# Kernel optimization log

Measured on AMD Instinct MI355X. Metric: run time of the kernel, lower is better.

Reference implementation:

```python
import jax, jax.numpy as jnp
import numpy as np

B, N, C = 4, 2048, 1024
H = 16
D = C // H  # head_dim = 64
SCALE = D ** -0.5


def setup_inputs() -> dict:
    key = jax.random.key(0)
    ks = jax.random.split(key, 5)
    s = 0.02
    return {
        "x": jax.random.normal(ks[0], (B, N, C), dtype=jnp.float32),
        "wq": jax.random.normal(ks[1], (C, C), dtype=jnp.float32) * s,
        "wk": jax.random.normal(ks[2], (C, C), dtype=jnp.float32) * s,
        "wv": jax.random.normal(ks[3], (C, C), dtype=jnp.float32) * s,
        "wo": jax.random.normal(ks[4], (C, C), dtype=jnp.float32) * s,
        "bo": jnp.zeros((C,), dtype=jnp.float32),
    }


def reference(x, wq, wk, wv, wo, bo):
    # nn.Linear: y = x @ W^T (no bias for q/k/v since qkv_bias=False)
    b, n, c = x.shape
    q = (x @ wq.T).reshape(b, n, H, D).transpose(0, 2, 1, 3)  # [B,H,N,D]
    k = (x @ wk.T).reshape(b, n, H, D).transpose(0, 2, 1, 3)
    v = (x @ wv.T).reshape(b, n, H, D).transpose(0, 2, 1, 3)
    q = q * SCALE
    attn = jax.nn.softmax(jnp.einsum("bhnd,bhmd->bhnm", q, k), axis=-1)
    out = jnp.einsum("bhnm,bhmd->bhnd", attn, v)  # [B,H,N,D]
    out = out.transpose(0, 2, 1, 3).reshape(b, n, c)
    return out @ wo.T + bo
```

## Files before the change

kernel.cpp:

```cpp
#include <hip/hip_runtime.h>
#include <hip/hip_bf16.h>
#include <stdint.h>


#define GAS __attribute__((address_space(1)))
#define LAS __attribute__((address_space(3)))

typedef __attribute__((ext_vector_type(8))) short v8s;
typedef __attribute__((ext_vector_type(4))) float v4f;

__device__ __forceinline__ unsigned short f2bf(float f) {
  __hip_bfloat16 h = __float2bfloat16(f);
  return __builtin_bit_cast(unsigned short, h);
}

__device__ __forceinline__ float fexp2(float x) {
#if __has_builtin(__builtin_amdgcn_exp2f)
  return __builtin_amdgcn_exp2f(x);
#else
  return __expf(x * 0.6931471805599453f);
#endif
}

__device__ __forceinline__ void gld_lds16(const void* g, void* l) {
  __builtin_amdgcn_global_load_lds((GAS void*)(uintptr_t)g,
                                   (LAS void*)(uint32_t)(uintptr_t)l,
                                   16, 0, 0);
}

__global__ void cvt_f32_bf16(const float* __restrict__ src,
                             unsigned short* __restrict__ dst, int n4) {
  int i = blockIdx.x * blockDim.x + threadIdx.x;
  const int stride = gridDim.x * blockDim.x;
  for (; i < n4; i += stride) {
    float4 f = ((const float4*)src)[i];
    ushort4 u;
    u.x = f2bf(f.x); u.y = f2bf(f.y); u.z = f2bf(f.z); u.w = f2bf(f.w);
    ((ushort4*)dst)[i] = u;
  }
}

template<int OUTMODE>
__global__ __launch_bounds__(256)
void gemm_bt(const unsigned short* __restrict__ A,
             const unsigned short* __restrict__ Bm,
             void* __restrict__ Cout, const float* __restrict__ bias,
             int M, int N, int K, int scaleCols, float scaleVal)
{
  __shared__ unsigned short sA[128 * 64];
  __shared__ unsigned short sB[128 * 64];

  const int tid  = threadIdx.x;
  const int lane = tid & 63;
  const int w    = tid >> 6;
  const int g    = lane >> 4;
  const int r16  = lane & 15;
  const long bm  = (long)blockIdx.y * 128;
  const long bn  = (long)blockIdx.x * 128;
  const int  wm  = (w >> 1) * 64;
  const int  wn  = (w & 1) * 64;

  v4f acc[4][4] = {};

  for (int k0 = 0; k0 < K; k0 += 64) {
    #pragma unroll
    for (int t4 = 0; t4 < 4; ++t4) {
      const int t   = t4 * 4 + w;
      const int row = t * 8 + (lane >> 3);
      const long co = (long)k0 + (lane & 7) * 8;
      gld_lds16(A  + (bm + row) * K + co, (char*)sA + t * 1024);
      gld_lds16(Bm + (bn + row) * K + co, (char*)sB + t * 1024);
    }
    __syncthreads();

    v8s af[4][2], bf[4][2];
    #pragma unroll
    for (int m = 0; m < 4; ++m)
      #pragma unroll
      for (int kk = 0; kk < 2; ++kk)
        af[m][kk] = *(const v8s*)(sA + (wm + m*16 + r16)*64 + kk*32 + g*8);
    #pragma unroll
    for (int n = 0; n < 4; ++n)
      #pragma unroll
      for (int kk = 0; kk < 2; ++kk)
        bf[n][kk] = *(const v8s*)(sB + (wn + n*16 + r16)*64 + kk*32 + g*8);
    #pragma unroll
    for (int kk = 0; kk < 2; ++kk)
      #pragma unroll
      for (int m = 0; m < 4; ++m)
        #pragma unroll
        for (int n = 0; n < 4; ++n)
          acc[m][n] = __builtin_amdgcn_mfma_f32_16x16x32_bf16(
              af[m][kk], bf[n][kk], acc[m][n], 0, 0, 0);
    __syncthreads();
  }

  #pragma unroll
  for (int m = 0; m < 4; ++m) {
    #pragma unroll
    for (int n = 0; n < 4; ++n) {
      const long row0 = bm + wm + m*16 + g*4;
      const long col  = bn + wn + n*16 + r16;
      if constexpr (OUTMODE == 0) {
        unsigned short* Cb = (unsigned short*)Cout;
        const float sc = (col < scaleCols) ? scaleVal : 1.0f;
        #pragma unroll
        for (int r = 0; r < 4; ++r)
          Cb[(row0 + r) * N + col] = f2bf(acc[m][n][r] * sc);
      } else {
        float* Cf = (float*)Cout;
        const float bv = bias[col];
        #pragma unroll
        for (int r = 0; r < 4; ++r)
          Cf[(row0 + r) * N + col] = acc[m][n][r] + bv;
      }
    }
  }
}

__global__ __launch_bounds__(256)
void attn_fwd(const unsigned short* __restrict__ Qkv,
              unsigned short* __restrict__ O)
{
  __shared__ unsigned short sK[2][128 * 64];
  __shared__ unsigned int   sVT32[2][64 * 64];
  __shared__ unsigned short sP[4][16 * 128];

  const int tid  = threadIdx.x;
  const int lane = tid & 63;
  const int w    = tid >> 6;
  const int g    = lane >> 4;
  const int r16  = lane & 15;
  const int b  = blockIdx.z;
  const int h  = blockIdx.y;
  const int qb = blockIdx.x;
  const long kvbase = (long)b * 2048;
  const long qrow0w = kvbase + qb * 64 + w * 16;
  const int ld = 3072;

  const int  rowk = w * 8 + (lane >> 3);
  const int  csrc = (lane & 7) ^ ((lane >> 3) & 7);
  const unsigned short* Kb = Qkv + 1024 + h*64 + csrc*8;
  const int  jp = lane, d0v = w * 16;
  const unsigned short* Vb = Qkv + 2048 + h*64 + d0v;

  v8s qf[2];
  #pragma unroll
  for (int kk = 0; kk < 2; ++kk)
    qf[kk] = *(const v8s*)(Qkv + (qrow0w + r16) * ld + h*64 + kk*32 + g*8);

  v4f oacc[4] = {};
  float mrow[4], lsum[4];
  #pragma unroll
  for (int r = 0; r < 4; ++r) { mrow[r] = -__builtin_inff(); lsum[r] = 0.0f; }

  v8s vreg[4];
  #pragma unroll
  for (int t4 = 0; t4 < 4; ++t4)
    gld_lds16(Kb + (kvbase + t4*32 + rowk) * ld,
              (char*)sK[0] + (t4*4 + w) * 1024);
  {
    const unsigned short* vs = Vb + (kvbase + 2*jp) * ld;
    vreg[0] = *(const v8s*)vs;
    vreg[1] = *(const v8s*)(vs + 8);
    vreg[2] = *(const v8s*)(vs + ld);
    vreg[3] = *(const v8s*)(vs + ld + 8);
  }

  for (int t = 0; t < 16; ++t) {
    unsigned short* sKc  = &sK[t & 1][0];
    unsigned int*   sVTc = &sVT32[t & 1][0];
    const unsigned short* sVTe = (const unsigned short*)sVTc;

    asm volatile("s_waitcnt vmcnt(0)" ::: "memory");
    #pragma unroll
    for (int e = 0; e < 8; ++e) {
      int d = d0v + e;
      sVTc[d*64 + (((jp >> 2) ^ (d & 15)) << 2) + (jp & 3)] =
          ((unsigned)(unsigned short)vreg[2][e] << 16) | (unsigned short)vreg[0][e];
      d = d0v + 8 + e;
      sVTc[d*64 + (((jp >> 2) ^ (d & 15)) << 2) + (jp & 3)] =
          ((unsigned)(unsigned short)vreg[3][e] << 16) | (unsigned short)vreg[1][e];
    }
    __syncthreads();

    if (t < 15) {
      const long kvn = kvbase + (long)(t + 1) * 128;
      char* sKn = (char*)&sK[(t + 1) & 1][0];
      #pragma unroll
      for (int t4 = 0; t4 < 4; ++t4)
        gld_lds16(Kb + (kvn + t4*32 + rowk) * ld, sKn + (t4*4 + w) * 1024);
      const unsigned short* vs = Vb + (kvn + 2*jp) * ld;
      vreg[0] = *(const v8s*)vs;
      vreg[1] = *(const v8s*)(vs + 8);
      vreg[2] = *(const v8s*)(vs + ld);
      vreg[3] = *(const v8s*)(vs + ld + 8);
    }

    v4f sacc[8] = {};
    __builtin_amdgcn_s_setprio(1);
    #pragma unroll
    for (int n = 0; n < 8; ++n) {
      const int row = n*16 + r16;
      v8s k0 = *(const v8s*)(sKc + row*64 + ((g ^ (row & 7)) << 3));
      v8s k1 = *(const v8s*)(sKc + row*64 + (((4 + g) ^ (row & 7)) << 3));
      sacc[n] = __builtin_amdgcn_mfma_f32_16x16x32_bf16(qf[0], k0, sacc[n], 0, 0, 0);
      sacc[n] = __builtin_amdgcn_mfma_f32_16x16x32_bf16(qf[1], k1, sacc[n], 0, 0, 0);
    }
    __builtin_amdgcn_s_setprio(0);

    float mx[4];
    #pragma unroll
    for (int r = 0; r < 4; ++r) {
      float v = fmaxf(fmaxf(fmaxf(sacc[0][r], sacc[1][r]),
                            fmaxf(sacc[2][r], sacc[3][r])),
                      fmaxf(fmaxf(sacc[4][r], sacc[5][r]),
                            fmaxf(sacc[6][r], sacc[7][r])));
      v = fmaxf(v, __shfl_xor(v, 1));
      v = fmaxf(v, __shfl_xor(v, 2));
      v = fmaxf(v, __shfl_xor(v, 4));
      v = fmaxf(v, __shfl_xor(v, 8));
      mx[r] = v;
    }
    const float need = fmaxf(fmaxf(mx[0] - mrow[0], mx[1] - mrow[1]),
                             fmaxf(mx[2] - mrow[2], mx[3] - mrow[3]));
    if (__any(need > 8.0f)) {
      #pragma unroll
      for (int r = 0; r < 4; ++r) {
        const float mnew  = fmaxf(mrow[r], mx[r]);
        const float alpha = fexp2(mrow[r] - mnew);
        mrow[r] = mnew;
        lsum[r] *= alpha;
        #pragma unroll
        for (int n = 0; n < 4; ++n) oacc[n][r] *= alpha;
      }
    }
    #pragma unroll
    for (int n = 0; n < 8; ++n)
      #pragma unroll
      for (int r = 0; r < 4; ++r) {
        const float p = fexp2(sacc[n][r] - mrow[r]);
        sacc[n][r] = p;
        lsum[r] += p;
      }

    unsigned short* pb = &sP[w][0];
    #pragma unroll
    for (int n = 0; n < 8; ++n) {
      const int col = n*16 + r16;
      const int ch  = col >> 3;
      #pragma unroll
      for (int r = 0; r < 4; ++r) {
        const int row = g*4 + r;
        pb[row*128 + ((ch ^ row) << 3) + (col & 7)] = f2bf(sacc[n][r]);
      }
    }

    __builtin_amdgcn_s_setprio(1);
    #pragma unroll
    for (int kk = 0; kk < 4; ++kk) {
      v8s pf = *(const v8s*)(pb + r16*128 + (((kk*4 + g) ^ r16) << 3));
      #pragma unroll
      for (int n = 0; n < 4; ++n) {
        const int d = n*16 + r16;
        v8s vf = *(const v8s*)(sVTe + d*128 + (((kk*4 + g) ^ (d & 15)) << 3));
        oacc[n] = __builtin_amdgcn_mfma_f32_16x16x32_bf16(pf, vf, oacc[n], 0, 0, 0);
      }
    }
    __builtin_amdgcn_s_setprio(0);
  }

  float rs[4];
  #pragma unroll
  for (int r = 0; r < 4; ++r) {
    float s = lsum[r];
    s += __shfl_xor(s, 1);
    s += __shfl_xor(s, 2);
    s += __shfl_xor(s, 4);
    s += __shfl_xor(s, 8);
    rs[r] = 1.0f / s;
  }
  #pragma unroll
  for (int n = 0; n < 4; ++n) {
    const int col = h*64 + n*16 + r16;
    #pragma unroll
    for (int r = 0; r < 4; ++r)
      O[(qrow0w + g*4 + r) * 1024 + col] = f2bf(oacc[n][r] * rs[r]);
  }
}

extern "C" void kernel_launch(void* const* d_in, const int* in_sizes, int n_in,
                              void* d_out, int out_size, void* d_ws, size_t ws_size,
                              hipStream_t stream)
{
  const float* x  = (const float*)d_in[0];
  const float* wq = (const float*)d_in[1];
  const float* wk = (const float*)d_in[2];
  const float* wv = (const float*)d_in[3];
  const float* wo = (const float*)d_in[4];
  const float* bo = (const float*)d_in[5];

  unsigned short* Xb   = (unsigned short*)d_ws;
  unsigned short* Wqkv = Xb   + (size_t)8192 * 1024;
  unsigned short* Wob  = Wqkv + (size_t)3072 * 1024;
  unsigned short* Qkv  = Wob  + (size_t)1024 * 1024;
  unsigned short* Obuf = Xb;
  float* out = (float*)d_out;

  cvt_f32_bf16<<<2048, 256, 0, stream>>>(x,  Xb,   8192 * 1024 / 4);
  cvt_f32_bf16<<<512,  256, 0, stream>>>(wq, Wqkv,              1024 * 1024 / 4);
  cvt_f32_bf16<<<512,  256, 0, stream>>>(wk, Wqkv + 1024*1024,  1024 * 1024 / 4);
  cvt_f32_bf16<<<512,  256, 0, stream>>>(wv, Wqkv + 2*1024*1024,1024 * 1024 / 4);
  cvt_f32_bf16<<<512,  256, 0, stream>>>(wo, Wob,               1024 * 1024 / 4);

  gemm_bt<0><<<dim3(24, 64), 256, 0, stream>>>(Xb, Wqkv, Qkv, nullptr,
                                               8192, 3072, 1024, 1024,
                                               0.18033688011112042f);
  attn_fwd<<<dim3(32, 16, 4), 256, 0, stream>>>(Qkv, Obuf);
  gemm_bt<1><<<dim3(8, 64), 256, 0, stream>>>(Obuf, Wob, out, bo,
                                              8192, 1024, 1024, 0, 1.0f);
}
```

Baseline: 383.7 us.

## Switch attention to 32x32x16 MFMA with transposed scores and register-resident P

Rewrites the attention kernel so each wave owns 32 query rows and computes S^T = K·Q^T with 32x32x16 bf16 MFMAs. The probability tile then stays in registers and is repacked with cvt_pk and a cross-half shuffle, so the LDS P buffer and its store/load round trip go away. Each block now covers 128 queries, which halves the grid and doubles K/V reuse per load. The cost is higher register pressure from v16f accumulators, and the unswizzled K layout in LDS may cause bank conflicts.

```diff
diff --git a/kernel.cpp b/kernel.cpp
--- a/kernel.cpp
+++ b/kernel.cpp
@@ -6,8 +6,9 @@
 #define GAS __attribute__((address_space(1)))
 #define LAS __attribute__((address_space(3)))
 
-typedef __attribute__((ext_vector_type(8))) short v8s;
-typedef __attribute__((ext_vector_type(4))) float v4f;
+typedef __attribute__((ext_vector_type(8)))  short v8s;
+typedef __attribute__((ext_vector_type(4)))  float v4f;
+typedef __attribute__((ext_vector_type(16))) float v16f;
 
 __device__ __forceinline__ unsigned short f2bf(float f) {
   __hip_bfloat16 h = __float2bfloat16(f);
@@ -20,6 +21,12 @@
 #else
   return __expf(x * 0.6931471805599453f);
 #endif
+}
+
+__device__ __forceinline__ unsigned cvtpk(float lo, float hi) {
+  unsigned r;
+  asm("v_cvt_pk_bf16_f32 %0, %1, %2" : "=v"(r) : "v"(lo), "v"(hi));
+  return r;
 }
 
 __device__ __forceinline__ void gld_lds16(const void* g, void* l) {
@@ -124,42 +131,38 @@
 {
   __shared__ unsigned short sK[2][128 * 64];
   __shared__ unsigned int   sVT32[2][64 * 64];
-  __shared__ unsigned short sP[4][16 * 128];
 
   const int tid  = threadIdx.x;
   const int lane = tid & 63;
   const int w    = tid >> 6;
-  const int g    = lane >> 4;
-  const int r16  = lane & 15;
+  const int l31  = lane & 31;
+  const int hi   = lane >> 5;
   const int b  = blockIdx.z;
   const int h  = blockIdx.y;
   const int qb = blockIdx.x;
   const long kvbase = (long)b * 2048;
-  const long qrow0w = kvbase + qb * 64 + w * 16;
-  const int ld = 3072;
-
-  const int  rowk = w * 8 + (lane >> 3);
-  const int  csrc = (lane & 7) ^ ((lane >> 3) & 7);
-  const unsigned short* Kb = Qkv + 1024 + h*64 + csrc*8;
-  const int  jp = lane, d0v = w * 16;
+  const int  ld = 3072;
+  const long qrow = kvbase + qb * 128 + w * 32 + l31;
+
+  v8s qf[4];
+  #pragma unroll
+  for (int s = 0; s < 4; ++s)
+    qf[s] = *(const v8s*)(Qkv + qrow * ld + h*64 + s*16 + hi*8);
+
+  const unsigned short* KsrcB = Qkv + (kvbase + w*32 + l31) * ld + 1024 + h*64 + hi*8;
+  const int jp = lane, d0v = w * 16;
   const unsigned short* Vb = Qkv + 2048 + h*64 + d0v;
 
-  v8s qf[2];
-  #pragma unroll
-  for (int kk = 0; kk < 2; ++kk)
-    qf[kk] = *(const v8s*)(Qkv + (qrow0w + r16) * ld + h*64 + kk*32 + g*8);
-
-  v4f oacc[4] = {};
-  float mrow[4], lsum[4];
-  #pragma unroll
-  for (int r = 0; r < 4; ++r) { mrow[r] = -__builtin_inff(); lsum[r] = 0.0f; }
+  v16f  oacc[2] = {};
+  float mrow = -__builtin_inff();
+  float lsum = 0.0f;
 
   v8s vreg[4];
-  #pragma unroll
-  for (int t4 = 0; t4 < 4; ++t4)
-    gld_lds16(Kb + (kvbase + t4*32 + rowk) * ld,
-              (char*)sK[0] + (t4*4 + w) * 1024);
   {
+    char* dK = (char*)&sK[0][0] + w * 4096;
+    #pragma unroll
+    for (int i = 0; i < 4; ++i)
+      gld_lds16(KsrcB + i * 16, dK + i * 1024);
     const unsigned short* vs = Vb + (kvbase + 2*jp) * ld;
     vreg[0] = *(const v8s*)vs;
     vreg[1] = *(const v8s*)(vs + 8);
@@ -168,8 +171,8 @@
   }
 
   for (int t = 0; t < 16; ++t) {
-    unsigned short* sKc  = &sK[t & 1][0];
-    unsigned int*   sVTc = &sVT32[t & 1][0];
+    const unsigned short* sKc = &sK[t & 1][0];
+    unsigned int* sVTc = &sVT32[t & 1][0];
     const unsigned short* sVTe = (const unsigned short*)sVTc;
 
     asm volatile("s_waitcnt vmcnt(0)" ::: "memory");
@@ -185,107 +188,112 @@
     __syncthreads();
 
     if (t < 15) {
-      const long kvn = kvbase + (long)(t + 1) * 128;
-      char* sKn = (char*)&sK[(t + 1) & 1][0];
-      #pragma unroll
-      for (int t4 = 0; t4 < 4; ++t4)
-        gld_lds16(Kb + (kvn + t4*32 + rowk) * ld, sKn + (t4*4 + w) * 1024);
-      const unsigned short* vs = Vb + (kvn + 2*jp) * ld;
+      const long kv0 = (long)(t + 1) * 128;
+      char* dK = (char*)&sK[(t + 1) & 1][0] + w * 4096;
+      #pragma unroll
+      for (int i = 0; i < 4; ++i)
+        gld_lds16(KsrcB + kv0 * ld + i * 16, dK + i * 1024);
+      const unsigned short* vs = Vb + (kvbase + kv0 + 2*jp) * ld;
       vreg[0] = *(const v8s*)vs;
       vreg[1] = *(const v8s*)(vs + 8);
       vreg[2] = *(const v8s*)(vs + ld);
       vreg[3] = *(const v8s*)(vs + ld + 8);
     }
 
-    v4f sacc[8] = {};
+    v16f sacc[4] = {};
     __builtin_amdgcn_s_setprio(1);
     #pragma unroll
-    for (int n = 0; n < 8; ++n) {
-      const int row = n*16 + r16;
-      v8s k0 = *(const v8s*)(sKc + row*64 + ((g ^ (row & 7)) << 3));
-      v8s k1 = *(const v8s*)(sKc + row*64 + (((4 + g) ^ (row & 7)) << 3));
-      sacc[n] = __builtin_amdgcn_mfma_f32_16x16x32_bf16(qf[0], k0, sacc[n], 0, 0, 0);
-      sacc[n] = __builtin_amdgcn_mfma_f32_16x16x32_bf16(qf[1], k1, sacc[n], 0, 0, 0);
-    }
+    for (int n = 0; n < 4; ++n)
+      #pragma unroll
+      for (int s = 0; s < 4; ++s) {
+        v8s kf = *(const v8s*)(sKc + (n*4 + s) * 512 + lane * 8);
+        sacc[n] = __builtin_amdgcn_mfma_f32_32x32x16_bf16(kf, qf[s], sacc[n], 0, 0, 0);
+      }
     __builtin_amdgcn_s_setprio(0);
 
-    float mx[4];
-    #pragma unroll
-    for (int r = 0; r < 4; ++r) {
-      float v = fmaxf(fmaxf(fmaxf(sacc[0][r], sacc[1][r]),
-                            fmaxf(sacc[2][r], sacc[3][r])),
-                      fmaxf(fmaxf(sacc[4][r], sacc[5][r]),
-                            fmaxf(sacc[6][r], sacc[7][r])));
-      v = fmaxf(v, __shfl_xor(v, 1));
-      v = fmaxf(v, __shfl_xor(v, 2));
-      v = fmaxf(v, __shfl_xor(v, 4));
-      v = fmaxf(v, __shfl_xor(v, 8));
-      mx[r] = v;
-    }
-    const float need = fmaxf(fmaxf(mx[0] - mrow[0], mx[1] - mrow[1]),
-                             fmaxf(mx[2] - mrow[2], mx[3] - mrow[3]));
-    if (__any(need > 8.0f)) {
-      #pragma unroll
-      for (int r = 0; r < 4; ++r) {
-        const float mnew  = fmaxf(mrow[r], mx[r]);
-        const float alpha = fexp2(mrow[r] - mnew);
-        mrow[r] = mnew;
-        lsum[r] *= alpha;
+    float red[16];
+    #pragma unroll
+    for (int j = 0; j < 16; ++j)
+      red[j] = fmaxf(fmaxf(sacc[0][j], sacc[1][j]),
+                     fmaxf(sacc[2][j], sacc[3][j]));
+    #pragma unroll
+    for (int off = 8; off >= 1; off >>= 1)
+      #pragma unroll
+      for (int j = 0; j < 8; ++j)
+        if (j < off) red[j] = fmaxf(red[j], red[j + off]);
+    const float mx = fmaxf(red[0], __shfl_xor(red[0], 32));
+
+    if (__any(mx - mrow > 8.0f)) {
+      const float mnew  = fmaxf(mrow, mx);
+      const float alpha = fexp2(mrow - mnew);
+      mrow = mnew;
+      lsum *= alpha;
+      #pragma unroll
+      for (int dg = 0; dg < 2; ++dg)
         #pragma unroll
-        for (int n = 0; n < 4; ++n) oacc[n][r] *= alpha;
+        for (int j = 0; j < 16; ++j)
+          oacc[dg][j] *= alpha;
+    }
+    {
+      float ls0 = 0.f, ls1 = 0.f, ls2 = 0.f, ls3 = 0.f;
+      #pragma unroll
+      for (int j = 0; j < 16; ++j) {
+        float p0 = fexp2(sacc[0][j] - mrow); sacc[0][j] = p0; ls0 += p0;
+        float p1 = fexp2(sacc[1][j] - mrow); sacc[1][j] = p1; ls1 += p1;
+        float p2 = fexp2(sacc[2][j] - mrow); sacc[2][j] = p2; ls2 += p2;
+        float p3 = fexp2(sacc[3][j] - mrow); sacc[3][j] = p3; ls3 += p3;
       }
-    }
-    #pragma unroll
-    for (int n = 0; n < 8; ++n)
-      #pragma unroll
-      for (int r = 0; r < 4; ++r) {
-        const float p = fexp2(sacc[n][r] - mrow[r]);
-        sacc[n][r] = p;
-        lsum[r] += p;
+      lsum += (ls0 + ls1) + (ls2 + ls3);
+    }
+
+    v8s pf[8];
+    #pragma unroll
+    for (int ks = 0; ks < 8; ++ks) {
+      const int n = ks >> 1, r0 = (ks & 1) * 8;
+      unsigned w0 = cvtpk(sacc[n][r0+0], sacc[n][r0+1]);
+      unsigned w1 = cvtpk(sacc[n][r0+2], sacc[n][r0+3]);
+      unsigned w2 = cvtpk(sacc[n][r0+4], sacc[n][r0+5]);
+      unsigned w3 = cvtpk(sacc[n][r0+6], sacc[n][r0+7]);
+      unsigned s0 = (unsigned)__shfl_xor((int)w0, 32);
+      unsigned s1 = (unsigned)__shfl_xor((int)w1, 32);
+      unsigned s2 = (unsigned)__shfl_xor((int)w2, 32);
+      unsigned s3 = (unsigned)__shfl_xor((int)w3, 32);
+      uint4 uu;
+      uu.x = hi ? s2 : w0;
+      uu.y = hi ? s3 : w1;
+      uu.z = hi ? w2 : s0;
+      uu.w = hi ? w3 : s1;
+      pf[ks] = __builtin_bit_cast(v8s, uu);
+    }
+
+    __builtin_amdgcn_s_setprio(1);
+    #pragma unroll
+    for (int dg = 0; dg < 2; ++dg) {
+      const int d = dg*32 + l31;
+      const unsigned short* vrow = sVTe + d*128;
+      #pragma unroll
+      for (int ks = 0; ks < 8; ++ks) {
+        v8s vf = *(const v8s*)(vrow + (((ks*2 + hi) ^ (d & 15)) << 3));
+        oacc[dg] = __builtin_amdgcn_mfma_f32_32x32x16_bf16(vf, pf[ks], oacc[dg], 0, 0, 0);
       }
-
-    unsigned short* pb = &sP[w][0];
-    #pragma unroll
-    for (int n = 0; n < 8; ++n) {
-      const int col = n*16 + r16;
-      const int ch  = col >> 3;
-      #pragma unroll
-      for (int r = 0; r < 4; ++r) {
-        const int row = g*4 + r;
-        pb[row*128 + ((ch ^ row) << 3) + (col & 7)] = f2bf(sacc[n][r]);
-      }
-    }
-
-    __builtin_amdgcn_s_setprio(1);
-    #pragma unroll
-    for (int kk = 0; kk < 4; ++kk) {
-      v8s pf = *(const v8s*)(pb + r16*128 + (((kk*4 + g) ^ r16) << 3));
-      #pragma unroll
-      for (int n = 0; n < 4; ++n) {
-        const int d = n*16 + r16;
-        v8s vf = *(const v8s*)(sVTe + d*128 + (((kk*4 + g) ^ (d & 15)) << 3));
-        oacc[n] = __builtin_amdgcn_mfma_f32_16x16x32_bf16(pf, vf, oacc[n], 0, 0, 0);
-      }
     }
     __builtin_amdgcn_s_setprio(0);
   }
 
-  float rs[4];
+  const float tot = lsum + __shfl_xor(lsum, 32);
+  const float inv = 1.0f / tot;
   #pragma unroll
-  for (int r = 0; r < 4; ++r) {
-    float s = lsum[r];
-    s += __shfl_xor(s, 1);
-    s += __shfl_xor(s, 2);
-    s += __shfl_xor(s, 4);
-    s += __shfl_xor(s, 8);
-    rs[r] = 1.0f / s;
-  }
-  #pragma unroll
-  for (int n = 0; n < 4; ++n) {
-    const int col = h*64 + n*16 + r16;
-    #pragma unroll
-    for (int r = 0; r < 4; ++r)
-      O[(qrow0w + g*4 + r) * 1024 + col] = f2bf(oacc[n][r] * rs[r]);
+  for (int dg = 0; dg < 2; ++dg) {
+    #pragma unroll
+    for (int rq = 0; rq < 4; ++rq) {
+      ushort4 pk4;
+      pk4.x = f2bf(oacc[dg][rq*4 + 0] * inv);
+      pk4.y = f2bf(oacc[dg][rq*4 + 1] * inv);
+      pk4.z = f2bf(oacc[dg][rq*4 + 2] * inv);
+      pk4.w = f2bf(oacc[dg][rq*4 + 3] * inv);
+      const int d0 = dg*32 + rq*8 + hi*4;
+      *(ushort4*)(O + qrow * 1024 + h*64 + d0) = pk4;
+    }
   }
 }
 
@@ -316,7 +324,7 @@
   gemm_bt<0><<<dim3(24, 64), 256, 0, stream>>>(Xb, Wqkv, Qkv, nullptr,
                                                8192, 3072, 1024, 1024,
                                                0.18033688011112042f);
-  attn_fwd<<<dim3(32, 16, 4), 256, 0, stream>>>(Qkv, Obuf);
+  attn_fwd<<<dim3(16, 16, 4), 256, 0, stream>>>(Qkv, Obuf);
   gemm_bt<1><<<dim3(8, 64), 256, 0, stream>>>(Obuf, Wob, out, bo,
                                               8192, 1024, 1024, 0, 1.0f);
 }
```

Result: slower. 398.1 us (+3.8%).
